# Optimization experiments

Measured on AMD Instinct MI355X. Metric: run time of the kernel, lower is better.

Reference implementation:

```python
import jax, jax.numpy as jnp
import numpy as np

B, D, NH, HD, L, P, FF = 2, 256, 8, 32, 4, 4, 1024
SPATIAL = np.array([[100, 100], [50, 50], [25, 25], [13, 13]], dtype=np.int64)
S_TOTAL = int(SPATIAL.prod(1).sum())  # 13294
EPS = 1e-5


def setup_inputs() -> dict:
    key = jax.random.key(0)
    ks = jax.random.split(key, 20)
    std = 0.02
    f32 = jnp.float32
    return {
        "query": jax.random.normal(ks[0], (B, S_TOTAL, D), f32),
        "query_pos": jax.random.normal(ks[1], (B, S_TOTAL, D), f32),
        "valid_ratios": jnp.ones((B, L, 2), f32),
        "spatial_shapes": SPATIAL,
        "level_start_index": np.concatenate([[0], SPATIAL.prod(1).cumsum()[:-1]]).astype(np.int64),
        "W_off": jax.random.normal(ks[2], (D, NH * L * P * 2), f32) * std,
        "b_off": jax.random.normal(ks[3], (NH * L * P * 2,), f32) * std,
        "W_attn": jax.random.normal(ks[4], (D, NH * L * P), f32) * std,
        "b_attn": jax.random.normal(ks[5], (NH * L * P,), f32) * std,
        "W_val": jax.random.normal(ks[6], (D, D), f32) * std,
        "b_val": jnp.zeros((D,), f32),
        "W_out": jax.random.normal(ks[7], (D, D), f32) * std,
        "b_out": jnp.zeros((D,), f32),
        "ln1_g": jnp.ones((D,), f32),
        "ln1_b": jnp.zeros((D,), f32),
        "W1": jax.random.normal(ks[8], (D, FF), f32) * std,
        "b1": jnp.zeros((FF,), f32),
        "W2": jax.random.normal(ks[9], (FF, D), f32) * std,
        "b2": jnp.zeros((D,), f32),
        "ln2_g": jnp.ones((D,), f32),
        "ln2_b": jnp.zeros((D,), f32),
    }


def _layer_norm(x, g, b):
    m = x.mean(-1, keepdims=True)
    v = ((x - m) ** 2).mean(-1, keepdims=True)
    return (x - m) * jax.lax.rsqrt(v + EPS) * g + b


def _bilinear_sample(v, loc, H, W):
    # v: [B, NH, H*W, HD]; loc: [B, NH, S, P, 2] normalized to [0,1]
    # Matches F.grid_sample(bilinear, padding_mode='zeros', align_corners=False)
    x = loc[..., 0] * W - 0.5
    y = loc[..., 1] * H - 0.5
    x0 = jnp.floor(x)
    y0 = jnp.floor(y)
    lx, ly = x - x0, y - y0
    x0i = x0.astype(jnp.int32)
    y0i = y0.astype(jnp.int32)
    x1i, y1i = x0i + 1, y0i + 1

    def corner(yi, xi, w):
        valid = (xi >= 0) & (xi < W) & (yi >= 0) & (yi < H)
        idx = jnp.clip(yi, 0, H - 1) * W + jnp.clip(xi, 0, W - 1)  # [B,NH,S,P]
        b_, h_, s_, p_ = idx.shape
        g = jnp.take_along_axis(v, idx.reshape(b_, h_, s_ * p_)[..., None], axis=2)
        g = g.reshape(b_, h_, s_, p_, -1)
        return g * (w * valid)[..., None]

    return (corner(y0i, x0i, (1 - lx) * (1 - ly)) + corner(y0i, x1i, lx * (1 - ly))
            + corner(y1i, x0i, (1 - lx) * ly) + corner(y1i, x1i, lx * ly))


def _forward(query, query_pos, valid_ratios, spatial_shapes,
             W_off, b_off, W_attn, b_attn, W_val, b_val, W_out, b_out,
             ln1_g, ln1_b, W1, b1, W2, b2, ln2_g, ln2_b):
    ss = np.asarray(spatial_shapes)
    Bq, S, _ = query.shape

    # ----- reference points (per-pixel centers, normalized by valid ratios) -----
    refs = []
    for lvl in range(ss.shape[0]):
        H, W = int(ss[lvl, 0]), int(ss[lvl, 1])
        ry, rx = jnp.meshgrid(jnp.linspace(0.5, H - 0.5, H), jnp.linspace(0.5, W - 0.5, W), indexing='ij')
        vy = valid_ratios[:, lvl, 1][:, None, None]
        vx = valid_ratios[:, lvl, 0][:, None, None]
        ry = ry[None] / (vy * H)
        rx = rx[None] / (vx * W)
        refs.append(jnp.stack((rx, ry), -1).reshape(Bq, H * W, 2))
    ref = jnp.concatenate(refs, 1)  # [B, S, 2] (identical across levels)

    # ----- multi-scale deformable attention -----
    q = query + query_pos
    v = (query @ W_val + b_val).reshape(Bq, S, NH, HD).transpose(0, 2, 1, 3)  # [B,NH,S,HD]
    off = (q @ W_off + b_off).reshape(Bq, S, NH, L, P, 2)
    aw = jax.nn.softmax((q @ W_attn + b_attn).reshape(Bq, S, NH, L * P), -1)
    aw = aw.reshape(Bq, S, NH, L, P)
    normalizer = jnp.asarray(ss[:, ::-1].copy(), jnp.float32)  # (W, H) per level
    loc = ref[:, :, None, None, None, :] + off / normalizer[None, None, None, :, None, :]  # [B,S,NH,L,P,2]

    starts = np.concatenate([[0], ss.prod(1).cumsum()[:-1]])
    out = jnp.zeros((Bq, NH, S, HD), query.dtype)
    for lvl in range(ss.shape[0]):
        H, W = int(ss[lvl, 0]), int(ss[lvl, 1])
        s0 = int(starts[lvl])
        v_l = v[:, :, s0:s0 + H * W]                       # [B,NH,HW,HD]
        loc_l = loc[:, :, :, lvl].transpose(0, 2, 1, 3, 4)  # [B,NH,S,P,2]
        samp = _bilinear_sample(v_l, loc_l, H, W)           # [B,NH,S,P,HD]
        w_l = aw[:, :, :, lvl].transpose(0, 2, 1, 3)        # [B,NH,S,P]
        out = out + (samp * w_l[..., None]).sum(3)
    attn_out = out.transpose(0, 2, 1, 3).reshape(Bq, S, D) @ W_out + b_out

    # ----- residual + LN + FFN + residual + LN -----
    x = _layer_norm(query + attn_out, ln1_g, ln1_b)
    f = jax.nn.relu(x @ W1 + b1) @ W2 + b2
    return _layer_norm(x + f, ln2_g, ln2_b)


def reference(query, query_pos, valid_ratios, spatial_shapes, level_start_index,
              W_off, b_off, W_attn, b_attn, W_val, b_val, W_out, b_out,
              ln1_g, ln1_b, W1, b1, W2, b2, ln2_g, ln2_b):
    return _forward(query, query_pos, valid_ratios, spatial_shapes,
                    W_off, b_off, W_attn, b_attn, W_val, b_val, W_out, b_out,
                    ln1_g, ln1_b, W1, b1, W2, b2, ln2_g, ln2_b)
```

## Files before the change

### kernel.cpp

```cpp
#include <hip/hip_runtime.h>
#include <math.h>

#define R_ROWS 26588
#define S_TOT  13294
#define NHEAD  8
#define NLVL   4
#define EPSF   1e-5f

typedef __attribute__((ext_vector_type(8))) short short8;
typedef __attribute__((ext_vector_type(4))) float f32x4;
typedef __attribute__((ext_vector_type(2))) float f32x2;
typedef unsigned short ushort_t;

__device__ __forceinline__ unsigned short f2bf(float f) {
    unsigned int u = __builtin_bit_cast(unsigned int, f);
    unsigned int r = (u + 0x7FFFu + ((u >> 16) & 1u)) >> 16;
    return (unsigned short)r;
}

__global__ __launch_bounds__(256) void transpose_all_kernel(
    const float* __restrict__ W_val, const float* __restrict__ W_off,
    const float* __restrict__ W_attn, const float* __restrict__ W_out,
    const float* __restrict__ W1, const float* __restrict__ W2,
    ushort_t* __restrict__ wt_val, ushort_t* __restrict__ wt_off,
    ushort_t* __restrict__ wt_attn, ushort_t* __restrict__ wt_out,
    ushort_t* __restrict__ wt_w1, ushort_t* __restrict__ wt_w2)
{
    int bid = blockIdx.x;
    const float* src; ushort_t* dst; int K, N, t;
    if (bid < 64)       { src = W_val;  dst = wt_val;  K = 256;  N = 256;  t = bid; }
    else if (bid < 128) { src = W_off;  dst = wt_off;  K = 256;  N = 256;  t = bid - 64; }
    else if (bid < 160) { src = W_attn; dst = wt_attn; K = 256;  N = 128;  t = bid - 128; }
    else if (bid < 224) { src = W_out;  dst = wt_out;  K = 256;  N = 256;  t = bid - 160; }
    else if (bid < 480) { src = W1;     dst = wt_w1;   K = 256;  N = 1024; t = bid - 224; }
    else                { src = W2;     dst = wt_w2;   K = 1024; N = 256;  t = bid - 480; }
    int nt = N / 32;
    int bn = (t % nt) * 32, bk = (t / nt) * 32;

    __shared__ ushort_t tt[32][33];
    int x = threadIdx.x & 31;
    int y = threadIdx.x >> 5;
#pragma unroll
    for (int i = 0; i < 4; ++i) {
        int k = y + i * 8;
        tt[x][k] = f2bf(src[(long)(bk + k) * N + bn + x]);
    }
    __syncthreads();
#pragma unroll
    for (int i = 0; i < 4; ++i) {
        int n = y + i * 8;
        dst[(long)(bn + n) * K + bk + x] = tt[n][x];
    }
}

__global__ __launch_bounds__(256) void addcvt_kernel(
    const float* __restrict__ q, const float* __restrict__ p,
    ushort_t* __restrict__ qry_bf, ushort_t* __restrict__ qsum_bf, int n4)
{
    int i = blockIdx.x * 256 + threadIdx.x;
    if (i >= n4) return;
    float4 a = ((const float4*)q)[i];
    float4 b = ((const float4*)p)[i];
    uint2 qa, qs;
    qa.x = (unsigned)f2bf(a.x) | ((unsigned)f2bf(a.y) << 16);
    qa.y = (unsigned)f2bf(a.z) | ((unsigned)f2bf(a.w) << 16);
    qs.x = (unsigned)f2bf(a.x + b.x) | ((unsigned)f2bf(a.y + b.y) << 16);
    qs.y = (unsigned)f2bf(a.z + b.z) | ((unsigned)f2bf(a.w + b.w) << 16);
    ((uint2*)qry_bf)[i] = qa;
    ((uint2*)qsum_bf)[i] = qs;
}

#define TBUF 4096

__device__ __forceinline__ void stage_ab(
    const ushort_t* __restrict__ Arow, const ushort_t* __restrict__ Brow,
    int K, int k0, ushort_t* As, ushort_t* Bs, int wave, int lane)
{
    int quadS = lane & 3;
    int rr = lane >> 2;
#pragma unroll
    for (int inst = 0; inst < 2; ++inst) {
        int base_row = wave * 32 + inst * 16;
        int r = base_row + rr;
        int quadG = quadS ^ ((r >> 1) & 3);
        const ushort_t* gp = Arow + (long)r * K + k0 + quadG * 8;
        __builtin_amdgcn_global_load_lds(
            (const __attribute__((address_space(1))) unsigned int*)gp,
            (__attribute__((address_space(3))) unsigned int*)&As[base_row * 32],
            16, 0, 0);
    }
#pragma unroll
    for (int inst = 0; inst < 2; ++inst) {
        int base_row = wave * 32 + inst * 16;
        int r = base_row + rr;
        int quadG = quadS ^ ((r >> 1) & 3);
        const ushort_t* gp = Brow + (long)r * K + k0 + quadG * 8;
        __builtin_amdgcn_global_load_lds(
            (const __attribute__((address_space(1))) unsigned int*)gp,
            (__attribute__((address_space(3))) unsigned int*)&Bs[base_row * 32],
            16, 0, 0);
    }
}

__device__ __forceinline__ void gemm_body(
    ushort_t* As, ushort_t* Bs,
    const ushort_t* __restrict__ A, const ushort_t* __restrict__ Wt,
    const float* __restrict__ bias, void* __restrict__ Cv,
    int M, int N, int K, int bm, int bn, bool out_bf16, bool relu)
{
    const int tid  = threadIdx.x;
    const int wave = tid >> 6;
    const int lane = tid & 63;
    const int l15  = lane & 15;
    const int quad = lane >> 4;
    const int wm   = (wave >> 1) * 64;
    const int wn   = (wave & 1) * 64;

    const ushort_t* Arow = A + (long)bm * K;
    const ushort_t* Brow = Wt + (long)bn * K;

    f32x4 acc[4][4];
#pragma unroll
    for (int i = 0; i < 4; ++i)
#pragma unroll
        for (int j = 0; j < 4; ++j) acc[i][j] = (f32x4)0.0f;

    int aoff[4], boff[4];
#pragma unroll
    for (int mi = 0; mi < 4; ++mi) {
        int r = wm + mi * 16 + l15;
        aoff[mi] = r * 32 + (quad ^ ((r >> 1) & 3)) * 8;
    }
#pragma unroll
    for (int ni = 0; ni < 4; ++ni) {
        int r = wn + ni * 16 + l15;
        boff[ni] = r * 32 + (quad ^ ((r >> 1) & 3)) * 8;
    }

    const int NT = K >> 5;
    stage_ab(Arow, Brow, K, 0, As, Bs, wave, lane);
    int cur = 0;
    for (int t = 0; t < NT; ++t) {
        int nxt = cur + 1; if (nxt == 3) nxt = 0;
        if (t + 1 < NT) {
            stage_ab(Arow, Brow, K, (t + 1) << 5,
                     As + nxt * TBUF, Bs + nxt * TBUF, wave, lane);
            asm volatile("s_waitcnt vmcnt(4)" ::: "memory");
        } else {
            asm volatile("s_waitcnt vmcnt(0)" ::: "memory");
        }
        asm volatile("s_barrier" ::: "memory");

        const ushort_t* Ab = As + cur * TBUF;
        const ushort_t* Bb = Bs + cur * TBUF;
        short8 af[4], bf[4];
#pragma unroll
        for (int mi = 0; mi < 4; ++mi) af[mi] = *(const short8*)&Ab[aoff[mi]];
#pragma unroll
        for (int ni = 0; ni < 4; ++ni) bf[ni] = *(const short8*)&Bb[boff[ni]];
#pragma unroll
        for (int mi = 0; mi < 4; ++mi)
#pragma unroll
            for (int ni = 0; ni < 4; ++ni)
                acc[mi][ni] = __builtin_amdgcn_mfma_f32_16x16x32_bf16(
                    af[mi], bf[ni], acc[mi][ni], 0, 0, 0);
        cur = nxt;
    }

#pragma unroll
    for (int mi = 0; mi < 4; ++mi) {
#pragma unroll
        for (int r = 0; r < 4; ++r) {
            int row = bm + wm + mi * 16 + quad * 4 + r;
            if (row >= M) continue;
#pragma unroll
            for (int ni = 0; ni < 4; ++ni) {
                int col = bn + wn + ni * 16 + l15;
                float vv = acc[mi][ni][r] + bias[col];
                if (relu) vv = fmaxf(vv, 0.f);
                if (out_bf16)
                    ((ushort_t*)Cv)[(long)row * N + col] = f2bf(vv);
                else
                    ((float*)Cv)[(long)row * N + col] = vv;
            }
        }
    }
}

template<bool OUT_BF16, bool RELU>
__global__ __launch_bounds__(256) void gemm_mfma_kernel(
    const ushort_t* __restrict__ A, const ushort_t* __restrict__ Wt,
    const float* __restrict__ bias, void* __restrict__ Cv,
    int M, int N, int K)
{
    __shared__ ushort_t As[3 * TBUF];
    __shared__ ushort_t Bs[3 * TBUF];
    gemm_body(As, Bs, A, Wt, bias, Cv, M, N, K,
              blockIdx.x * 128, blockIdx.y * 128, OUT_BF16, RELU);
}

__global__ __launch_bounds__(256) void proj_kernel(
    const ushort_t* __restrict__ qry_bf, const ushort_t* __restrict__ q_bf,
    const ushort_t* __restrict__ wt_val, const ushort_t* __restrict__ wt_off,
    const ushort_t* __restrict__ wt_attn,
    const float* __restrict__ b_val, const float* __restrict__ b_off,
    const float* __restrict__ b_attn,
    ushort_t* __restrict__ v_bf, float* __restrict__ cb, float* __restrict__ logits)
{
    __shared__ ushort_t As[3 * TBUF];
    __shared__ ushort_t Bs[3 * TBUF];
    int y = blockIdx.y;
    const ushort_t* A; const ushort_t* Wt; const float* bias;
    void* C; bool outbf; int N, bn;
    if (y < 2)      { A = qry_bf; Wt = wt_val;  bias = b_val;  C = v_bf;   outbf = true;  N = 256; bn = y * 128; }
    else if (y < 4) { A = q_bf;   Wt = wt_off;  bias = b_off;  C = cb;     outbf = false; N = 256; bn = (y - 2) * 128; }
    else            { A = q_bf;   Wt = wt_attn; bias = b_attn; C = logits; outbf = false; N = 128; bn = 0; }
    gemm_body(As, Bs, A, Wt, bias, C, R_ROWS, N, 256, blockIdx.x * 128, bn, outbf, false);
}

#define DEF_BLOCKS 3328
#define DEF_CHUNK  416

__global__ __launch_bounds__(256) void deform_sample_kernel(
    const ushort_t* __restrict__ v, const float* __restrict__ off,
    const float* __restrict__ logits, const float* __restrict__ vr,
    ushort_t* __restrict__ out)
{
    const int Hs_[4] = {100, 50, 25, 13};
    const int S0_[4] = {0, 10000, 12500, 13125};

    int wb  = (blockIdx.x & 7) * DEF_CHUNK + (blockIdx.x >> 3);
    int grp = wb * 64 + (threadIdx.x >> 2);
    int j   = threadIdx.x & 3;
    if (grp >= R_ROWS * NHEAD) return;
    int h = grp & 7;
    int r = grp >> 3;
    int b = (r >= S_TOT) ? 1 : 0;
    int s = r - b * S_TOT;

    int lq = (s < 10000) ? 0 : (s < 12500) ? 1 : (s < 13125) ? 2 : 3;
    int t  = s - S0_[lq];
    int Wq = Hs_[lq];
    int iy = t / Wq;
    int jx = t - iy * Wq;
    float vx = vr[(b * NLVL + lq) * 2 + 0];
    float vy = vr[(b * NLVL + lq) * 2 + 1];
    float rx = (jx + 0.5f) / (vx * (float)Wq);
    float ry = (iy + 0.5f) / (vy * (float)Wq);

    const float* offp = off + (long)r * 256 + h * 32;
    float4 oa = ((const float4*)offp)[2 * j];
    float4 ob = ((const float4*)offp)[2 * j + 1];
    float4 lg = ((const float4*)(logits + (long)grp * 16))[j];

    float mx = fmaxf(fmaxf(lg.x, lg.y), fmaxf(lg.z, lg.w));
    mx = fmaxf(mx, __shfl_xor(mx, 1));
    mx = fmaxf(mx, __shfl_xor(mx, 2));
    float e0 = __expf(lg.x - mx), e1 = __expf(lg.y - mx);
    float e2 = __expf(lg.z - mx), e3 = __expf(lg.w - mx);
    float sum = e0 + e1 + e2 + e3;
    sum += __shfl_xor(sum, 1);
    sum += __shfl_xor(sum, 2);
    float inv = 1.f / sum;

    const int   H  = Hs_[j];
    const float fH = (float)H;
    const int   s0 = S0_[j];
    float oxs[4] = {oa.x, oa.z, ob.x, ob.z};
    float oys[4] = {oa.y, oa.w, ob.y, ob.w};
    float wts[4] = {e0 * inv, e1 * inv, e2 * inv, e3 * inv};
    float pw0[4], pw1[4], pw2[4], pw3[4];
    int   pi0[4], pi1[4], pi2[4], pi3[4];
#pragma unroll
    for (int i = 0; i < 4; ++i) {
        float x = rx * fH + oxs[i] - 0.5f;
        float y = ry * fH + oys[i] - 0.5f;
        float xf = floorf(x), yf = floorf(y);
        float lx = x - xf, ly = y - yf;
        int x0 = (int)xf, y0 = (int)yf;
        bool xv0 = (x0 >= 0) & (x0 < H);
        bool xv1 = (x0 >= -1) & (x0 < H - 1);
        bool yv0 = (y0 >= 0) & (y0 < H);
        bool yv1 = (y0 >= -1) & (y0 < H - 1);
        float w = wts[i];
        pw0[i] = (xv0 & yv0) ? (1.f - lx) * (1.f - ly) * w : 0.f;
        pw1[i] = (xv1 & yv0) ? lx * (1.f - ly) * w : 0.f;
        pw2[i] = (xv0 & yv1) ? (1.f - lx) * ly * w : 0.f;
        pw3[i] = (xv1 & yv1) ? lx * ly * w : 0.f;
        int xc0 = min(max(x0, 0), H - 1), xc1 = min(max(x0 + 1, 0), H - 1);
        int yc0 = min(max(y0, 0), H - 1), yc1 = min(max(y0 + 1, 0), H - 1);
        pi0[i] = s0 + yc0 * H + xc0;
        pi1[i] = s0 + yc0 * H + xc1;
        pi2[i] = s0 + yc1 * H + xc0;
        pi3[i] = s0 + yc1 * H + xc1;
    }

    const ushort_t* vb = v + ((long)b * S_TOT) * 256 + h * 32 + j * 8;
    f32x2 acc2[4];
#pragma unroll
    for (int c = 0; c < 4; ++c) acc2[c] = (f32x2)0.0f;

#define ACC_CORNER(IDX, WGT) do {                                            \
        uint4 g = *(const uint4*)&vb[(long)(IDX) * 256];                     \
        unsigned uu0 = g.x, uu1 = g.y, uu2 = g.z, uu3 = g.w;                 \
        f32x2 gv;                                                            \
        gv.x = __builtin_bit_cast(float, uu0 << 16);                         \
        gv.y = __builtin_bit_cast(float, uu0 & 0xFFFF0000u);                 \
        acc2[0] += gv * (WGT);                                               \
        gv.x = __builtin_bit_cast(float, uu1 << 16);                         \
        gv.y = __builtin_bit_cast(float, uu1 & 0xFFFF0000u);                 \
        acc2[1] += gv * (WGT);                                               \
        gv.x = __builtin_bit_cast(float, uu2 << 16);                         \
        gv.y = __builtin_bit_cast(float, uu2 & 0xFFFF0000u);                 \
        acc2[2] += gv * (WGT);                                               \
        gv.x = __builtin_bit_cast(float, uu3 << 16);                         \
        gv.y = __builtin_bit_cast(float, uu3 & 0xFFFF0000u);                 \
        acc2[3] += gv * (WGT);                                               \
    } while (0)

#pragma unroll
    for (int i = 0; i < 4; ++i) {
#pragma unroll
        for (int j2 = 0; j2 < 4; ++j2) {
            float w00 = __shfl(pw0[i], j2, 4);
            float w01 = __shfl(pw1[i], j2, 4);
            float w10 = __shfl(pw2[i], j2, 4);
            float w11 = __shfl(pw3[i], j2, 4);
            int   i00 = __shfl(pi0[i], j2, 4);
            int   i01 = __shfl(pi1[i], j2, 4);
            int   i10 = __shfl(pi2[i], j2, 4);
            int   i11 = __shfl(pi3[i], j2, 4);
            ACC_CORNER(i00, w00);
            ACC_CORNER(i01, w01);
            ACC_CORNER(i10, w10);
            ACC_CORNER(i11, w11);
        }
    }
#undef ACC_CORNER

    uint4 o;
    o.x = (unsigned)f2bf(acc2[0].x) | ((unsigned)f2bf(acc2[0].y) << 16);
    o.y = (unsigned)f2bf(acc2[1].x) | ((unsigned)f2bf(acc2[1].y) << 16);
    o.z = (unsigned)f2bf(acc2[2].x) | ((unsigned)f2bf(acc2[2].y) << 16);
    o.w = (unsigned)f2bf(acc2[3].x) | ((unsigned)f2bf(acc2[3].y) << 16);
    *(uint4*)&out[(long)r * 256 + h * 32 + j * 8] = o;
}

template<bool DUAL>
__global__ __launch_bounds__(256) void add_ln_kernel(
    const float* __restrict__ a, const float* __restrict__ b,
    const float* __restrict__ g, const float* __restrict__ beta,
    float* __restrict__ outf, ushort_t* __restrict__ outb)
{
    int row = blockIdx.x;
    int tid = threadIdx.x;
    float x = a[(long)row * 256 + tid] + b[(long)row * 256 + tid];
    float s1 = x, s2 = x * x;
#pragma unroll
    for (int o = 32; o > 0; o >>= 1) {
        s1 += __shfl_down(s1, o, 64);
        s2 += __shfl_down(s2, o, 64);
    }
    __shared__ float sh1[4], sh2[4];
    int w = tid >> 6;
    if ((tid & 63) == 0) { sh1[w] = s1; sh2[w] = s2; }
    __syncthreads();
    float t1 = sh1[0] + sh1[1] + sh1[2] + sh1[3];
    float t2 = sh2[0] + sh2[1] + sh2[2] + sh2[3];
    float mean = t1 * (1.f / 256.f);
    float var  = t2 * (1.f / 256.f) - mean * mean;
    float inv  = rsqrtf(var + EPSF);
    float y = (x - mean) * inv * g[tid] + beta[tid];
    outf[(long)row * 256 + tid] = y;
    if (DUAL) outb[(long)row * 256 + tid] = f2bf(y);
}

extern "C" void kernel_launch(void* const* d_in, const int* in_sizes, int n_in,
                              void* d_out, int out_size, void* d_ws, size_t ws_size,
                              hipStream_t stream)
{
    const float* query  = (const float*)d_in[0];
    const float* qpos   = (const float*)d_in[1];
    const float* vr     = (const float*)d_in[2];
    const float* W_off  = (const float*)d_in[5];
    const float* b_off  = (const float*)d_in[6];
    const float* W_attn = (const float*)d_in[7];
    const float* b_attn = (const float*)d_in[8];
    const float* W_val  = (const float*)d_in[9];
    const float* b_val  = (const float*)d_in[10];
    const float* W_out  = (const float*)d_in[11];
    const float* b_out  = (const float*)d_in[12];
    const float* ln1g   = (const float*)d_in[13];
    const float* ln1b   = (const float*)d_in[14];
    const float* W1     = (const float*)d_in[15];
    const float* b1     = (const float*)d_in[16];
    const float* W2     = (const float*)d_in[17];
    const float* b2     = (const float*)d_in[18];
    const float* ln2g   = (const float*)d_in[19];
    const float* ln2b   = (const float*)d_in[20];
    float* out = (float*)d_out;

    float* ws = (float*)d_ws;
    const long R128 = (long)R_ROWS * 128;
    ushort_t* q_bf    = (ushort_t*)(ws);
    ushort_t* qry_bf  = (ushort_t*)(ws + R128);
    ushort_t* v_bf    = (ushort_t*)(ws + 2 * R128);
    float*    logits  = ws + 3 * R128;
    ushort_t* h_bf    = (ushort_t*)(ws);
    float*    cb      = ws + 4 * R128;
    ushort_t* samp_bf = (ushort_t*)(ws + 6 * R128);
    float*    xb      = ws + 7 * R128;
    ushort_t* wt      = (ushort_t*)(ws + 9 * R128);
    ushort_t* wt_val  = wt;
    ushort_t* wt_off  = wt + 65536;
    ushort_t* wt_attn = wt + 131072;
    ushort_t* wt_out  = wt + 163840;
    ushort_t* wt_w1   = wt + 229376;
    ushort_t* wt_w2   = wt + 491520;

    dim3 blk(256);
    const int MB = (R_ROWS + 127) / 128;

    transpose_all_kernel<<<736, blk, 0, stream>>>(
        W_val, W_off, W_attn, W_out, W1, W2,
        wt_val, wt_off, wt_attn, wt_out, wt_w1, wt_w2);
    addcvt_kernel<<<(R_ROWS * 64 + 255) / 256, blk, 0, stream>>>(
        query, qpos, qry_bf, q_bf, R_ROWS * 64);
    proj_kernel<<<dim3(MB, 5), blk, 0, stream>>>(
        qry_bf, q_bf, wt_val, wt_off, wt_attn, b_val, b_off, b_attn,
        v_bf, cb, logits);
    deform_sample_kernel<<<DEF_BLOCKS, blk, 0, stream>>>(
        v_bf, cb, logits, vr, samp_bf);
    gemm_mfma_kernel<false, false><<<dim3(MB, 2), blk, 0, stream>>>(
        samp_bf, wt_out, b_out, cb, R_ROWS, 256, 256);
    add_ln_kernel<true><<<R_ROWS, blk, 0, stream>>>(query, cb, ln1g, ln1b, xb, samp_bf);
    gemm_mfma_kernel<true, true><<<dim3(MB, 8), blk, 0, stream>>>(
        samp_bf, wt_w1, b1, h_bf, R_ROWS, 1024, 256);
    gemm_mfma_kernel<false, false><<<dim3(MB, 2), blk, 0, stream>>>(
        h_bf, wt_w2, b2, cb, R_ROWS, 256, 1024);
    add_ln_kernel<false><<<R_ROWS, blk, 0, stream>>>(xb, cb, ln2g, ln2b, out, nullptr);
}
```

Measured before the change: 326.9 us.

## Fuse residual add and LayerNorm into output GEMMs; merge prep kernels

```diff
diff --git a/kernel.cpp b/kernel.cpp
--- a/kernel.cpp
+++ b/kernel.cpp
@@ -18,59 +18,54 @@
     return (unsigned short)r;
 }
 
-__global__ __launch_bounds__(256) void transpose_all_kernel(
+__global__ __launch_bounds__(256) void prep_kernel(
     const float* __restrict__ W_val, const float* __restrict__ W_off,
     const float* __restrict__ W_attn, const float* __restrict__ W_out,
     const float* __restrict__ W1, const float* __restrict__ W2,
     ushort_t* __restrict__ wt_val, ushort_t* __restrict__ wt_off,
     ushort_t* __restrict__ wt_attn, ushort_t* __restrict__ wt_out,
-    ushort_t* __restrict__ wt_w1, ushort_t* __restrict__ wt_w2)
-{
+    ushort_t* __restrict__ wt_w1, ushort_t* __restrict__ wt_w2,
+    const float* __restrict__ query, const float* __restrict__ qpos,
+    ushort_t* __restrict__ qry_bf, ushort_t* __restrict__ qsum_bf)
+{
+    __shared__ ushort_t tt[32][33];
     int bid = blockIdx.x;
-    const float* src; ushort_t* dst; int K, N, t;
-    if (bid < 64)       { src = W_val;  dst = wt_val;  K = 256;  N = 256;  t = bid; }
-    else if (bid < 128) { src = W_off;  dst = wt_off;  K = 256;  N = 256;  t = bid - 64; }
-    else if (bid < 160) { src = W_attn; dst = wt_attn; K = 256;  N = 128;  t = bid - 128; }
-    else if (bid < 224) { src = W_out;  dst = wt_out;  K = 256;  N = 256;  t = bid - 160; }
-    else if (bid < 480) { src = W1;     dst = wt_w1;   K = 256;  N = 1024; t = bid - 224; }
-    else                { src = W2;     dst = wt_w2;   K = 1024; N = 256;  t = bid - 480; }
-    int nt = N / 32;
-    int bn = (t % nt) * 32, bk = (t / nt) * 32;
-
-    __shared__ ushort_t tt[32][33];
-    int x = threadIdx.x & 31;
-    int y = threadIdx.x >> 5;
-#pragma unroll
-    for (int i = 0; i < 4; ++i) {
-        int k = y + i * 8;
-        tt[x][k] = f2bf(src[(long)(bk + k) * N + bn + x]);
-    }
-    __syncthreads();
-#pragma unroll
-    for (int i = 0; i < 4; ++i) {
-        int n = y + i * 8;
-        dst[(long)(bn + n) * K + bk + x] = tt[n][x];
-    }
-}
-
-__global__ __launch_bounds__(256) void addcvt_kernel(
-    const float* __restrict__ q, const float* __restrict__ p,
-    ushort_t* __restrict__ qry_bf, ushort_t* __restrict__ qsum_bf, int n4)
-{
-    int i = blockIdx.x * 256 + threadIdx.x;
-    if (i >= n4) return;
-    float4 a = ((const float4*)q)[i];
-    float4 b = ((const float4*)p)[i];
-    uint2 qa, qs;
-    qa.x = (unsigned)f2bf(a.x) | ((unsigned)f2bf(a.y) << 16);
-    qa.y = (unsigned)f2bf(a.z) | ((unsigned)f2bf(a.w) << 16);
-    qs.x = (unsigned)f2bf(a.x + b.x) | ((unsigned)f2bf(a.y + b.y) << 16);
-    qs.y = (unsigned)f2bf(a.z + b.z) | ((unsigned)f2bf(a.w + b.w) << 16);
-    ((uint2*)qry_bf)[i] = qa;
-    ((uint2*)qsum_bf)[i] = qs;
-}
-
-#define TBUF 4096
+    if (bid < 736) {
+        const float* src; ushort_t* dst; int K, N, t;
+        if (bid < 64)       { src = W_val;  dst = wt_val;  K = 256;  N = 256;  t = bid; }
+        else if (bid < 128) { src = W_off;  dst = wt_off;  K = 256;  N = 256;  t = bid - 64; }
+        else if (bid < 160) { src = W_attn; dst = wt_attn; K = 256;  N = 128;  t = bid - 128; }
+        else if (bid < 224) { src = W_out;  dst = wt_out;  K = 256;  N = 256;  t = bid - 160; }
+        else if (bid < 480) { src = W1;     dst = wt_w1;   K = 256;  N = 1024; t = bid - 224; }
+        else                { src = W2;     dst = wt_w2;   K = 1024; N = 256;  t = bid - 480; }
+        int nt = N / 32;
+        int bn = (t % nt) * 32, bk = (t / nt) * 32;
+        int x = threadIdx.x & 31;
+        int y = threadIdx.x >> 5;
+#pragma unroll
+        for (int i = 0; i < 4; ++i) {
+            int k = y + i * 8;
+            tt[x][k] = f2bf(src[(long)(bk + k) * N + bn + x]);
+        }
+        __syncthreads();
+#pragma unroll
+        for (int i = 0; i < 4; ++i) {
+            int n = y + i * 8;
+            dst[(long)(bn + n) * K + bk + x] = tt[n][x];
+        }
+    } else {
+        int i = (bid - 736) * 256 + threadIdx.x;
+        float4 a = ((const float4*)query)[i];
+        float4 b = ((const float4*)qpos)[i];
+        uint2 qa, qs;
+        qa.x = (unsigned)f2bf(a.x) | ((unsigned)f2bf(a.y) << 16);
+        qa.y = (unsigned)f2bf(a.z) | ((unsigned)f2bf(a.w) << 16);
+        qs.x = (unsigned)f2bf(a.x + b.x) | ((unsigned)f2bf(a.y + b.y) << 16);
+        qs.y = (unsigned)f2bf(a.z + b.z) | ((unsigned)f2bf(a.w + b.w) << 16);
+        ((uint2*)qry_bf)[i] = qa;
+        ((uint2*)qsum_bf)[i] = qs;
+    }
+}
 
 __device__ __forceinline__ void stage_ab(
     const ushort_t* __restrict__ Arow, const ushort_t* __restrict__ Brow,
@@ -144,15 +139,15 @@
         int nxt = cur + 1; if (nxt == 3) nxt = 0;
         if (t + 1 < NT) {
             stage_ab(Arow, Brow, K, (t + 1) << 5,
-                     As + nxt * TBUF, Bs + nxt * TBUF, wave, lane);
+                     As + nxt * 4096, Bs + nxt * 4096, wave, lane);
             asm volatile("s_waitcnt vmcnt(4)" ::: "memory");
         } else {
             asm volatile("s_waitcnt vmcnt(0)" ::: "memory");
         }
         asm volatile("s_barrier" ::: "memory");
 
-        const ushort_t* Ab = As + cur * TBUF;
-        const ushort_t* Bb = Bs + cur * TBUF;
+        const ushort_t* Ab = As + cur * 4096;
+        const ushort_t* Bb = Bs + cur * 4096;
         short8 af[4], bf[4];
 #pragma unroll
         for (int mi = 0; mi < 4; ++mi) af[mi] = *(const short8*)&Ab[aoff[mi]];
@@ -193,8 +188,8 @@
     const float* __restrict__ bias, void* __restrict__ Cv,
     int M, int N, int K)
 {
-    __shared__ ushort_t As[3 * TBUF];
-    __shared__ ushort_t Bs[3 * TBUF];
+    __shared__ ushort_t As[3 * 4096];
+    __shared__ ushort_t Bs[3 * 4096];
     gemm_body(As, Bs, A, Wt, bias, Cv, M, N, K,
               blockIdx.x * 128, blockIdx.y * 128, OUT_BF16, RELU);
 }
@@ -207,8 +202,8 @@
     const float* __restrict__ b_attn,
     ushort_t* __restrict__ v_bf, float* __restrict__ cb, float* __restrict__ logits)
 {
-    __shared__ ushort_t As[3 * TBUF];
-    __shared__ ushort_t Bs[3 * TBUF];
+    __shared__ ushort_t As[3 * 4096];
+    __shared__ ushort_t Bs[3 * 4096];
     int y = blockIdx.y;
     const ushort_t* A; const ushort_t* Wt; const float* bias;
     void* C; bool outbf; int N, bn;
@@ -216,6 +211,172 @@
     else if (y < 4) { A = q_bf;   Wt = wt_off;  bias = b_off;  C = cb;     outbf = false; N = 256; bn = (y - 2) * 128; }
     else            { A = q_bf;   Wt = wt_attn; bias = b_attn; C = logits; outbf = false; N = 128; bn = 0; }
     gemm_body(As, Bs, A, Wt, bias, C, R_ROWS, N, 256, blockIdx.x * 128, bn, outbf, false);
+}
+
+__device__ __forceinline__ void stage_ln(
+    const ushort_t* __restrict__ Arow, const ushort_t* __restrict__ Brow,
+    int K, int k0, ushort_t* As, ushort_t* Bs, int wave, int lane)
+{
+    int quadS = lane & 3;
+    int rr = lane >> 2;
+    if (wave < 2) {
+        int base_row = wave * 16;
+        int r = base_row + rr;
+        int quadG = quadS ^ ((r >> 1) & 3);
+        const ushort_t* gp = Arow + (long)r * K + k0 + quadG * 8;
+        __builtin_amdgcn_global_load_lds(
+            (const __attribute__((address_space(1))) unsigned int*)gp,
+            (__attribute__((address_space(3))) unsigned int*)&As[base_row * 32],
+            16, 0, 0);
+    }
+#pragma unroll
+    for (int inst = 0; inst < 4; ++inst) {
+        int base_row = wave * 64 + inst * 16;
+        int r = base_row + rr;
+        int quadG = quadS ^ ((r >> 1) & 3);
+        const ushort_t* gp = Brow + (long)r * K + k0 + quadG * 8;
+        __builtin_amdgcn_global_load_lds(
+            (const __attribute__((address_space(1))) unsigned int*)gp,
+            (__attribute__((address_space(3))) unsigned int*)&Bs[base_row * 32],
+            16, 0, 0);
+    }
+}
+
+template<bool DUAL>
+__global__ __launch_bounds__(256) void gemm_ln_kernel(
+    const ushort_t* __restrict__ A, const ushort_t* __restrict__ Wt,
+    const float* __restrict__ bias, const float* __restrict__ resid,
+    const float* __restrict__ gam, const float* __restrict__ bet,
+    float* __restrict__ outf, ushort_t* __restrict__ outb,
+    int M, int K)
+{
+    __shared__ ushort_t As[3 * 1024];
+    __shared__ ushort_t Bs[3 * 8192];
+    __shared__ float s1s[32][4], s2s[32][4];
+
+    const int tid  = threadIdx.x;
+    const int wave = tid >> 6;
+    const int lane = tid & 63;
+    const int l15  = lane & 15;
+    const int quad = lane >> 4;
+    const int wn   = wave * 64;
+    const int bm   = blockIdx.x * 32;
+
+    const ushort_t* Arow = A + (long)bm * K;
+
+    float bias4[4], g4[4], be4[4];
+#pragma unroll
+    for (int ni = 0; ni < 4; ++ni) {
+        int col = wn + ni * 16 + l15;
+        bias4[ni] = bias[col];
+        g4[ni]    = gam[col];
+        be4[ni]   = bet[col];
+    }
+    float rv[2][4][4];
+#pragma unroll
+    for (int mi = 0; mi < 2; ++mi)
+#pragma unroll
+        for (int rr = 0; rr < 4; ++rr) {
+            int row = bm + mi * 16 + quad * 4 + rr;
+#pragma unroll
+            for (int ni = 0; ni < 4; ++ni) {
+                int col = wn + ni * 16 + l15;
+                rv[mi][rr][ni] = (row < M) ? resid[(long)row * 256 + col] : 0.f;
+            }
+        }
+
+    f32x4 acc[2][4];
+#pragma unroll
+    for (int i = 0; i < 2; ++i)
+#pragma unroll
+        for (int j = 0; j < 4; ++j) acc[i][j] = (f32x4)0.0f;
+
+    int aoff[2], boff[4];
+#pragma unroll
+    for (int mi = 0; mi < 2; ++mi) {
+        int r = mi * 16 + l15;
+        aoff[mi] = r * 32 + (quad ^ ((r >> 1) & 3)) * 8;
+    }
+#pragma unroll
+    for (int ni = 0; ni < 4; ++ni) {
+        int r = wn + ni * 16 + l15;
+        boff[ni] = r * 32 + (quad ^ ((r >> 1) & 3)) * 8;
+    }
+
+    const int NT = K >> 5;
+    stage_ln(Arow, Wt, K, 0, As, Bs, wave, lane);
+    int cur = 0;
+    for (int t = 0; t < NT; ++t) {
+        int nxt = cur + 1; if (nxt == 3) nxt = 0;
+        if (t + 1 < NT) {
+            stage_ln(Arow, Wt, K, (t + 1) << 5,
+                     As + nxt * 1024, Bs + nxt * 8192, wave, lane);
+            asm volatile("s_waitcnt vmcnt(4)" ::: "memory");
+        } else {
+            asm volatile("s_waitcnt vmcnt(0)" ::: "memory");
+        }
+        asm volatile("s_barrier" ::: "memory");
+
+        const ushort_t* Ab = As + cur * 1024;
+        const ushort_t* Bb = Bs + cur * 8192;
+        short8 af[2], bf[4];
+#pragma unroll
+        for (int mi = 0; mi < 2; ++mi) af[mi] = *(const short8*)&Ab[aoff[mi]];
+#pragma unroll
+        for (int ni = 0; ni < 4; ++ni) bf[ni] = *(const short8*)&Bb[boff[ni]];
+#pragma unroll
+        for (int mi = 0; mi < 2; ++mi)
+#pragma unroll
+            for (int ni = 0; ni < 4; ++ni)
+                acc[mi][ni] = __builtin_amdgcn_mfma_f32_16x16x32_bf16(
+                    af[mi], bf[ni], acc[mi][ni], 0, 0, 0);
+        cur = nxt;
+    }
+
+#pragma unroll
+    for (int mi = 0; mi < 2; ++mi)
+#pragma unroll
+        for (int rr = 0; rr < 4; ++rr) {
+            float s1 = 0.f, s2 = 0.f;
+#pragma unroll
+            for (int ni = 0; ni < 4; ++ni) {
+                float x = acc[mi][ni][rr] + bias4[ni] + rv[mi][rr][ni];
+                acc[mi][ni][rr] = x;
+                s1 += x; s2 += x * x;
+            }
+#pragma unroll
+            for (int o = 1; o < 16; o <<= 1) {
+                s1 += __shfl_xor(s1, o);
+                s2 += __shfl_xor(s2, o);
+            }
+            if (l15 == 0) {
+                int rl = mi * 16 + quad * 4 + rr;
+                s1s[rl][wave] = s1;
+                s2s[rl][wave] = s2;
+            }
+        }
+    __syncthreads();
+#pragma unroll
+    for (int mi = 0; mi < 2; ++mi)
+#pragma unroll
+        for (int rr = 0; rr < 4; ++rr) {
+            int rl  = mi * 16 + quad * 4 + rr;
+            int row = bm + rl;
+            float t1 = s1s[rl][0] + s1s[rl][1] + s1s[rl][2] + s1s[rl][3];
+            float t2 = s2s[rl][0] + s2s[rl][1] + s2s[rl][2] + s2s[rl][3];
+            float mean = t1 * (1.f / 256.f);
+            float var  = t2 * (1.f / 256.f) - mean * mean;
+            float inv  = rsqrtf(var + EPSF);
+            if (row < M) {
+#pragma unroll
+                for (int ni = 0; ni < 4; ++ni) {
+                    int col = wn + ni * 16 + l15;
+                    float y = (acc[mi][ni][rr] - mean) * inv * g4[ni] + be4[ni];
+                    outf[(long)row * 256 + col] = y;
+                    if (DUAL) outb[(long)row * 256 + col] = f2bf(y);
+                }
+            }
+        }
 }
 
 #define DEF_BLOCKS 3328
@@ -346,35 +507,6 @@
     *(uint4*)&out[(long)r * 256 + h * 32 + j * 8] = o;
 }
 
-template<bool DUAL>
-__global__ __launch_bounds__(256) void add_ln_kernel(
-    const float* __restrict__ a, const float* __restrict__ b,
-    const float* __restrict__ g, const float* __restrict__ beta,
-    float* __restrict__ outf, ushort_t* __restrict__ outb)
-{
-    int row = blockIdx.x;
-    int tid = threadIdx.x;
-    float x = a[(long)row * 256 + tid] + b[(long)row * 256 + tid];
-    float s1 = x, s2 = x * x;
-#pragma unroll
-    for (int o = 32; o > 0; o >>= 1) {
-        s1 += __shfl_down(s1, o, 64);
-        s2 += __shfl_down(s2, o, 64);
-    }
-    __shared__ float sh1[4], sh2[4];
-    int w = tid >> 6;
-    if ((tid & 63) == 0) { sh1[w] = s1; sh2[w] = s2; }
-    __syncthreads();
-    float t1 = sh1[0] + sh1[1] + sh1[2] + sh1[3];
-    float t2 = sh2[0] + sh2[1] + sh2[2] + sh2[3];
-    float mean = t1 * (1.f / 256.f);
-    float var  = t2 * (1.f / 256.f) - mean * mean;
-    float inv  = rsqrtf(var + EPSF);
-    float y = (x - mean) * inv * g[tid] + beta[tid];
-    outf[(long)row * 256 + tid] = y;
-    if (DUAL) outb[(long)row * 256 + tid] = f2bf(y);
-}
-
 extern "C" void kernel_launch(void* const* d_in, const int* in_sizes, int n_in,
                               void* d_out, int out_size, void* d_ws, size_t ws_size,
                               hipStream_t stream)
@@ -419,24 +551,22 @@
     ushort_t* wt_w2   = wt + 491520;
 
     dim3 blk(256);
-    const int MB = (R_ROWS + 127) / 128;
-
-    transpose_all_kernel<<<736, blk, 0, stream>>>(
+    const int MB128 = (R_ROWS + 127) / 128;
+    const int MB32  = (R_ROWS + 31) / 32;
+
+    prep_kernel<<<736 + R_ROWS / 4, blk, 0, stream>>>(
         W_val, W_off, W_attn, W_out, W1, W2,
-        wt_val, wt_off, wt_attn, wt_out, wt_w1, wt_w2);
-    addcvt_kernel<<<(R_ROWS * 64 + 255) / 256, blk, 0, stream>>>(
-        query, qpos, qry_bf, q_bf, R_ROWS * 64);
-    proj_kernel<<<dim3(MB, 5), blk, 0, stream>>>(
+        wt_val, wt_off, wt_attn, wt_out, wt_w1, wt_w2,
+        query, qpos, qry_bf, q_bf);
+    proj_kernel<<<dim3(MB128, 5), blk, 0, stream>>>(
         qry_bf, q_bf, wt_val, wt_off, wt_attn, b_val, b_off, b_attn,
         v_bf, cb, logits);
     deform_sample_kernel<<<DEF_BLOCKS, blk, 0, stream>>>(
         v_bf, cb, logits, vr, samp_bf);
-    gemm_mfma_kernel<false, false><<<dim3(MB, 2), blk, 0, stream>>>(
-        samp_bf, wt_out, b_out, cb, R_ROWS, 256, 256);
-    add_ln_kernel<true><<<R_ROWS, blk, 0, stream>>>(query, cb, ln1g, ln1b, xb, samp_bf);
-    gemm_mfma_kernel<true, true><<<dim3(MB, 8), blk, 0, stream>>>(
+    gemm_ln_kernel<true><<<MB32, blk, 0, stream>>>(
+        samp_bf, wt_out, b_out, query, ln1g, ln1b, xb, samp_bf, R_ROWS, 256);
+    gemm_mfma_kernel<true, true><<<dim3(MB128, 8), blk, 0, stream>>>(
         samp_bf, wt_w1, b1, h_bf, R_ROWS, 1024, 256);
-    gemm_mfma_kernel<false, false><<<dim3(MB, 2), blk, 0, stream>>>(
-        h_bf, wt_w2, b2, cb, R_ROWS, 256, 1024);
-    add_ln_kernel<false><<<R_ROWS, blk, 0, stream>>>(xb, cb, ln2g, ln2b, out, nullptr);
-}
+    gemm_ln_kernel<false><<<MB32, blk, 0, stream>>>(
+        h_bf, wt_w2, b2, xb, ln2g, ln2b, out, nullptr, R_ROWS, 1024);
+}
```

After: 318.0 us. -2.7%, faster.
